# Kernel optimization log

Hardware: AMD Instinct MI355X
Metric: run time of the kernel (lower is better)

The kernel has to match this reference:

```python
import jax, jax.numpy as jnp
import numpy as np

N_NODES = 100000
N_EDGES = 600000
D = 128          # embedding_dim == hidden_dim
OUT = 128        # output_dim
L = 5            # number of GINConv layers


def setup_inputs() -> dict:
    key = jax.random.key(0)
    ks = jax.random.split(key, 9)
    return {
        "x": jax.random.randint(ks[0], (N_NODES,), 0, N_NODES),
        "edge_index": jax.random.randint(ks[1], (2, N_EDGES), 0, N_NODES),
        "emb": jax.random.normal(ks[2], (N_NODES, D), dtype=jnp.float32) * 0.02,
        "Wa": jax.random.normal(ks[3], (L, D, D), dtype=jnp.float32) * 0.05,
        "ba": jnp.zeros((L, D), dtype=jnp.float32),
        "Wb": jax.random.normal(ks[4], (L, D, D), dtype=jnp.float32) * 0.05,
        "bb": jnp.zeros((L, D), dtype=jnp.float32),
        "Wlin": jax.random.normal(ks[5], (D, OUT), dtype=jnp.float32) * 0.05,
        "blin": jnp.zeros((OUT,), dtype=jnp.float32),
    }


def reference(x, edge_index, emb, Wa, ba, Wb, bb, Wlin, blin):
    src, dst = edge_index[0], edge_index[1]
    h = emb[x]  # [N, D] embedding lookup
    for l in range(L):
        # GINConv with eps=0: mlp((1+eps)*x_i + sum_{j->i} x_j)
        agg = jax.ops.segment_sum(h[src], dst, num_segments=N_NODES)  # [N, D]
        z = h + agg
        z = jax.nn.relu(z @ Wa[l] + ba[l])  # MLP hidden
        z = z @ Wb[l] + bb[l]               # MLP out
        h = jax.nn.relu(z)                  # outer F.relu in forward
    pooled = jnp.sum(h, axis=0, keepdims=True)  # global_add_pool, batch=None -> [1, D]
    return pooled @ Wlin + blin                  # [1, OUT]
```

## Files before the change

kernel.cpp:

```cpp
#include <hip/hip_runtime.h>

#define D 128
#define NLAYERS 5

using short8  = __attribute__((ext_vector_type(8))) short;
using short4v = __attribute__((ext_vector_type(4))) short;
using floatx4 = __attribute__((ext_vector_type(4))) float;
using floatx2 = __attribute__((ext_vector_type(2))) float;

__device__ __forceinline__ unsigned bf16_rne(float x) {
    unsigned u = __float_as_uint(x);
    return (u + 0x7fffu + ((u >> 16) & 1u)) >> 16;
}
__device__ __forceinline__ float bf16_to_f32(short s) {
    return __uint_as_float(((unsigned)(unsigned short)s) << 16);
}

#define HSCALE 16.0f
#define HSCALE_INV 0.0625f

__global__ void prepA_kernel(const int* __restrict__ x, const float* __restrict__ emb,
                             const float* __restrict__ Wa, const float* __restrict__ Wb,
                             const int* __restrict__ edst,
                             unsigned char* __restrict__ H0, short* __restrict__ wt,
                             int* __restrict__ deg,
                             int n_nodes, int n_edges) {
    const int gtid = blockIdx.x * 256 + threadIdx.x;
    const int gsz  = gridDim.x * 256;
    for (int g = gtid; g < 2 * NLAYERS * D * D; g += gsz) {
        int mat = g >> 14, idx = g & 16383;
        int n = idx >> 7, k = idx & 127;
        const float* W = (mat & 1) ? (Wb + (size_t)(mat >> 1) * D * D)
                                   : (Wa + (size_t)(mat >> 1) * D * D);
        wt[g] = (short)bf16_rne(W[k * D + n]);
    }
    for (int t = gtid; t < n_nodes * 32; t += gsz) {
        int node = t >> 5, lane = t & 31;
        int s = x[node];
        const float4 v = *reinterpret_cast<const float4*>(emb + (size_t)s * D + lane * 4);
        int w = __builtin_amdgcn_cvt_pk_fp8_f32(v.x * HSCALE, v.y * HSCALE, 0, false);
        w = __builtin_amdgcn_cvt_pk_fp8_f32(v.z * HSCALE, v.w * HSCALE, w, true);
        reinterpret_cast<unsigned int*>(H0)[(size_t)node * 32 + lane] = (unsigned int)w;
    }
    for (int e = gtid; e < n_edges; e += gsz) atomicAdd(&deg[edst[e]], 1);
}

#define SCAN_TILE 1024
__global__ void scan_sums_kernel(const int* __restrict__ deg, int* __restrict__ bsums, int n) {
    __shared__ int red[256];
    int base = blockIdx.x * SCAN_TILE + threadIdx.x * 4;
    int s = 0;
    #pragma unroll
    for (int j = 0; j < 4; j++) {
        int i = base + j;
        if (i < n) s += deg[i];
    }
    red[threadIdx.x] = s;
    __syncthreads();
    for (int off = 128; off > 0; off >>= 1) {
        if (threadIdx.x < off) red[threadIdx.x] += red[threadIdx.x + off];
        __syncthreads();
    }
    if (threadIdx.x == 0) bsums[blockIdx.x] = red[0];
}

__global__ void scan_bsums_kernel(int* __restrict__ bsums, int nblocks) {
    __shared__ int sdata[256];
    int carry = 0;
    for (int base = 0; base < nblocks; base += 256) {
        int i = base + threadIdx.x;
        int v = (i < nblocks) ? bsums[i] : 0;
        sdata[threadIdx.x] = v;
        __syncthreads();
        for (int off = 1; off < 256; off <<= 1) {
            int t = (threadIdx.x >= off) ? sdata[threadIdx.x - off] : 0;
            __syncthreads();
            sdata[threadIdx.x] += t;
            __syncthreads();
        }
        int incl = sdata[threadIdx.x];
        if (i < nblocks) bsums[i] = carry + incl - v;
        carry += sdata[255];
        __syncthreads();
    }
}

__global__ void scan_final_kernel(const int* __restrict__ deg, const int* __restrict__ bsums,
                                  int* __restrict__ offsets, int* __restrict__ cursor, int n) {
    __shared__ int sdata[256];
    int base = blockIdx.x * SCAN_TILE + threadIdx.x * 4;
    int v[4];
    int s = 0;
    #pragma unroll
    for (int j = 0; j < 4; j++) {
        int i = base + j;
        v[j] = (i < n) ? deg[i] : 0;
        s += v[j];
    }
    sdata[threadIdx.x] = s;
    __syncthreads();
    for (int off = 1; off < 256; off <<= 1) {
        int t = (threadIdx.x >= off) ? sdata[threadIdx.x - off] : 0;
        __syncthreads();
        sdata[threadIdx.x] += t;
        __syncthreads();
    }
    int excl = sdata[threadIdx.x] - s + bsums[blockIdx.x];
    #pragma unroll
    for (int j = 0; j < 4; j++) {
        int i = base + j;
        if (i <= n) offsets[i] = excl;
        if (i < n) cursor[i] = excl;
        excl += v[j];
    }
}

__global__ void fill_kernel(const int* __restrict__ esrc, const int* __restrict__ edst,
                            int* __restrict__ cursor, int* __restrict__ csr_src, int n_edges) {
    int e = blockIdx.x * 256 + threadIdx.x;
    if (e >= n_edges) return;
    int pos = atomicAdd(&cursor[edst[e]], 1);
    csr_src[pos] = esrc[e];
}

__global__ __launch_bounds__(512, 6) void layer_kernel(
        const int* __restrict__ offsets, const int* __restrict__ csr_src,
        const unsigned char* __restrict__ h_in, const short* __restrict__ wta,
        const short* __restrict__ wtb, const float* __restrict__ ba,
        const float* __restrict__ bb, unsigned char* __restrict__ h_out,
        float* __restrict__ pooled_accum, int n_rows) {
    __shared__ __align__(16) short zsh[64 * 128];
    __shared__ __align__(16) short wsh[128 * 128];

    const int tid  = threadIdx.x;
    const int row0 = blockIdx.x * 64;

    #pragma unroll
    for (int i = 0; i < 4; i++) {
        int g = i * 512 + tid;
        int n = g >> 4, c = g & 15;
        int off = (n * 16 + (c ^ (n & 15))) * 8;
        *reinterpret_cast<short8*>(&wsh[off]) =
            *reinterpret_cast<const short8*>(wta + n * D + c * 8);
    }

    {
        const int r  = tid >> 3;
        const int l8 = tid & 7;
        const int gr = row0 + r;
        float acc[16];
        if (gr < n_rows) {
            {
                uint4 w = *reinterpret_cast<const uint4*>(h_in + (size_t)gr * D + l8 * 16);
                unsigned int wd[4] = {w.x, w.y, w.z, w.w};
                #pragma unroll
                for (int k = 0; k < 4; k++) {
                    floatx2 lo = __builtin_amdgcn_cvt_pk_f32_fp8((int)wd[k], false);
                    floatx2 hi = __builtin_amdgcn_cvt_pk_f32_fp8((int)wd[k], true);
                    acc[4 * k]     = lo[0]; acc[4 * k + 1] = lo[1];
                    acc[4 * k + 2] = hi[0]; acc[4 * k + 3] = hi[1];
                }
            }
            int beg = offsets[gr];
            int end = offsets[gr + 1];
            int e = beg;
            for (; e + 3 < end; e += 4) {
                int sA = csr_src[e];
                int sB = csr_src[e + 1];
                int sC = csr_src[e + 2];
                int sD = csr_src[e + 3];
                uint4 wA = *reinterpret_cast<const uint4*>(h_in + (size_t)sA * D + l8 * 16);
                uint4 wB = *reinterpret_cast<const uint4*>(h_in + (size_t)sB * D + l8 * 16);
                uint4 wC = *reinterpret_cast<const uint4*>(h_in + (size_t)sC * D + l8 * 16);
                uint4 wD = *reinterpret_cast<const uint4*>(h_in + (size_t)sD * D + l8 * 16);
                unsigned int da[4] = {wA.x, wA.y, wA.z, wA.w};
                unsigned int db[4] = {wB.x, wB.y, wB.z, wB.w};
                unsigned int dc[4] = {wC.x, wC.y, wC.z, wC.w};
                unsigned int dd[4] = {wD.x, wD.y, wD.z, wD.w};
                #pragma unroll
                for (int k = 0; k < 4; k++) {
                    floatx2 alo = __builtin_amdgcn_cvt_pk_f32_fp8((int)da[k], false);
                    floatx2 ahi = __builtin_amdgcn_cvt_pk_f32_fp8((int)da[k], true);
                    floatx2 blo = __builtin_amdgcn_cvt_pk_f32_fp8((int)db[k], false);
                    floatx2 bhi = __builtin_amdgcn_cvt_pk_f32_fp8((int)db[k], true);
                    floatx2 clo = __builtin_amdgcn_cvt_pk_f32_fp8((int)dc[k], false);
                    floatx2 chi = __builtin_amdgcn_cvt_pk_f32_fp8((int)dc[k], true);
                    floatx2 dlo = __builtin_amdgcn_cvt_pk_f32_fp8((int)dd[k], false);
                    floatx2 dhi = __builtin_amdgcn_cvt_pk_f32_fp8((int)dd[k], true);
                    acc[4 * k]     += (alo[0] + blo[0]) + (clo[0] + dlo[0]);
                    acc[4 * k + 1] += (alo[1] + blo[1]) + (clo[1] + dlo[1]);
                    acc[4 * k + 2] += (ahi[0] + bhi[0]) + (chi[0] + dhi[0]);
                    acc[4 * k + 3] += (ahi[1] + bhi[1]) + (chi[1] + dhi[1]);
                }
            }
            for (; e < end; e++) {
                int sA = csr_src[e];
                uint4 wA = *reinterpret_cast<const uint4*>(h_in + (size_t)sA * D + l8 * 16);
                unsigned int da[4] = {wA.x, wA.y, wA.z, wA.w};
                #pragma unroll
                for (int k = 0; k < 4; k++) {
                    floatx2 alo = __builtin_amdgcn_cvt_pk_f32_fp8((int)da[k], false);
                    floatx2 ahi = __builtin_amdgcn_cvt_pk_f32_fp8((int)da[k], true);
                    acc[4 * k]     += alo[0];
                    acc[4 * k + 1] += alo[1];
                    acc[4 * k + 2] += ahi[0];
                    acc[4 * k + 3] += ahi[1];
                }
            }
        } else {
            #pragma unroll
            for (int j = 0; j < 16; j++) acc[j] = 0.f;
        }
        short8 o0, o1;
        #pragma unroll
        for (int j = 0; j < 8; j++) {
            o0[j] = (short)bf16_rne(acc[j] * HSCALE_INV);
            o1[j] = (short)bf16_rne(acc[8 + j] * HSCALE_INV);
        }
        const int c0i = 2 * l8, c1i = 2 * l8 + 1;
        *reinterpret_cast<short8*>(&zsh[(r * 16 + (c0i ^ (r & 15))) * 8]) = o0;
        *reinterpret_cast<short8*>(&zsh[(r * 16 + (c1i ^ (r & 15))) * 8]) = o1;
    }
    __syncthreads();

    const int lane = tid & 63;
    const int wave = tid >> 6;
    const int wr   = wave >> 1;
    const int wc   = wave & 1;
    const int lm   = lane & 15;
    const int quad = lane >> 4;

    floatx4 acc1[4];
    #pragma unroll
    for (int b = 0; b < 4; b++) acc1[b] = floatx4{0.f, 0.f, 0.f, 0.f};
    {
        const int r = wr * 16 + lm;
        #pragma unroll
        for (int ks = 0; ks < 4; ks++) {
            const int c = ks * 4 + quad;
            short8 av = *reinterpret_cast<const short8*>(&zsh[(r * 16 + (c ^ (r & 15))) * 8]);
            #pragma unroll
            for (int cs = 0; cs < 4; cs++) {
                int nn = wc * 64 + cs * 16 + lm;
                short8 bv = *reinterpret_cast<const short8*>(&wsh[(nn * 16 + (c ^ (nn & 15))) * 8]);
                acc1[cs] = __builtin_amdgcn_mfma_f32_16x16x32_bf16(av, bv, acc1[cs], 0, 0, 0);
            }
        }
    }
    __syncthreads();

    #pragma unroll
    for (int i = 0; i < 4; i++) {
        int g = i * 512 + tid;
        int n = g >> 4, c = g & 15;
        int off = (n * 16 + (c ^ (n & 15))) * 8;
        *reinterpret_cast<short8*>(&wsh[off]) =
            *reinterpret_cast<const short8*>(wtb + n * D + c * 8);
    }

    #pragma unroll
    for (int cs = 0; cs < 4; cs++) {
        int col = wc * 64 + cs * 16 + lm;
        float bva = ba[col];
        int cj = col >> 3, ci = col & 7;
        #pragma unroll
        for (int reg = 0; reg < 4; reg++) {
            int r = wr * 16 + quad * 4 + reg;
            float v = fmaxf(acc1[cs][reg] + bva, 0.f);
            zsh[(r * 16 + (cj ^ (r & 15))) * 8 + ci] = (short)bf16_rne(v);
        }
    }
    __syncthreads();

    floatx4 acc2[4];
    #pragma unroll
    for (int b = 0; b < 4; b++) acc2[b] = floatx4{0.f, 0.f, 0.f, 0.f};
    {
        const int r = wr * 16 + lm;
        #pragma unroll
        for (int ks = 0; ks < 4; ks++) {
            const int c = ks * 4 + quad;
            short8 av = *reinterpret_cast<const short8*>(&zsh[(r * 16 + (c ^ (r & 15))) * 8]);
            #pragma unroll
            for (int cs = 0; cs < 4; cs++) {
                int nn = wc * 64 + cs * 16 + lm;
                short8 bv = *reinterpret_cast<const short8*>(&wsh[(nn * 16 + (c ^ (nn & 15))) * 8]);
                acc2[cs] = __builtin_amdgcn_mfma_f32_16x16x32_bf16(av, bv, acc2[cs], 0, 0, 0);
            }
        }
    }

    float psum[4];
    #pragma unroll
    for (int cs = 0; cs < 4; cs++) {
        int col = wc * 64 + cs * 16 + lm;
        float bvb = bb[col];
        float s = 0.f;
        #pragma unroll
        for (int reg = 0; reg < 4; reg++) {
            int r = row0 + wr * 16 + quad * 4 + reg;
            if (r < n_rows) {
                float v = fmaxf(acc2[cs][reg] + bvb, 0.f);
                if (h_out != nullptr) {
                    float sv = v * HSCALE;
                    int pw = __builtin_amdgcn_cvt_pk_fp8_f32(sv, sv, 0, false);
                    h_out[(size_t)r * D + col] = (unsigned char)(pw & 0xff);
                }
                s += v;
            }
        }
        psum[cs] = s;
    }

    if (pooled_accum != nullptr) {
        __syncthreads();
        float* part = (float*)zsh;
        #pragma unroll
        for (int cs = 0; cs < 4; cs++)
            part[(wr * 4 + quad) * 128 + wc * 64 + cs * 16 + lm] = psum[cs];
        __syncthreads();
        if (tid < 128) {
            float s = 0.f;
            #pragma unroll
            for (int g = 0; g < 16; g++) s += part[g * 128 + tid];
            atomicAdd(&pooled_accum[tid], s);
        }
    }
}

__global__ void final_kernel(const float* __restrict__ pooled, const float* __restrict__ Wlin,
                             const float* __restrict__ blin, float* __restrict__ out) {
    const int j = threadIdx.x;
    __shared__ float p[D];
    p[j] = pooled[j];
    __syncthreads();
    float s = blin[j];
    #pragma unroll 8
    for (int k = 0; k < D; k++) s += p[k] * Wlin[k * D + j];
    out[j] = s;
}

extern "C" void kernel_launch(void* const* d_in, const int* in_sizes, int n_in,
                              void* d_out, int out_size, void* d_ws, size_t ws_size,
                              hipStream_t stream) {
    const int*   x    = (const int*)d_in[0];
    const int*   ei   = (const int*)d_in[1];
    const float* emb  = (const float*)d_in[2];
    const float* Wa   = (const float*)d_in[3];
    const float* ba   = (const float*)d_in[4];
    const float* Wb   = (const float*)d_in[5];
    const float* bb   = (const float*)d_in[6];
    const float* Wlin = (const float*)d_in[7];
    const float* blin = (const float*)d_in[8];
    float* out = (float*)d_out;

    const int N = in_sizes[0];
    const int E = in_sizes[1] / 2;
    const int* esrc = ei;
    const int* edst = ei + E;

    unsigned char* H0 = (unsigned char*)d_ws;
    unsigned char* H1 = H0 + (size_t)N * D;
    float* pooled = (float*)(H1 + (size_t)N * D);
    int* deg     = (int*)(pooled + 128);
    int* offsets = deg + N;
    int* cursor  = offsets + (N + 1);
    int* bsums   = cursor + N;
    int* csr_src = bsums + 4096;
    uintptr_t wt_addr = ((uintptr_t)(csr_src + E) + 15) & ~(uintptr_t)15;
    short* wt = (short*)wt_addr;

    const int scan_blocks = (N + 1 + SCAN_TILE - 1) / SCAN_TILE;

    hipMemsetAsync(pooled, 0, (size_t)(128 + N) * sizeof(int), stream);

    prepA_kernel<<<1024, 256, 0, stream>>>(x, emb, Wa, Wb, edst, H0, wt, deg, N, E);
    scan_sums_kernel<<<scan_blocks, 256, 0, stream>>>(deg, bsums, N);
    scan_bsums_kernel<<<1, 256, 0, stream>>>(bsums, scan_blocks);
    scan_final_kernel<<<scan_blocks, 256, 0, stream>>>(deg, bsums, offsets, cursor, N);
    fill_kernel<<<(E + 255) / 256, 256, 0, stream>>>(esrc, edst, cursor, csr_src, E);

    const int layer_blocks = (N + 63) / 64;
    unsigned char* hin = H0; unsigned char* hout = H1;
    for (int l = 0; l < NLAYERS; l++) {
        const bool last = (l == NLAYERS - 1);
        float* pacc = last ? pooled : nullptr;
        unsigned char* hdst = last ? nullptr : hout;
        layer_kernel<<<layer_blocks, 512, 0, stream>>>(
            offsets, csr_src, hin,
            wt + (size_t)(2 * l) * D * D, wt + (size_t)(2 * l + 1) * D * D,
            ba + (size_t)l * D, bb + (size_t)l * D, hdst, pacc, N);
        unsigned char* tmp = hin; hin = hout; hout = tmp;
    }

    final_kernel<<<1, 128, 0, stream>>>(pooled, Wlin, blin, out);
}
```

Before: 379.2 us.

## Split fused layer kernel into separate aggregation and MLP kernels

Moves the neighbor gather-sum out of the fused layer kernel into its own lightweight kernel that writes swizzled bf16 rows to a global z buffer. The MLP kernel then loads those tiles straight into shared memory. The intent is to let the latency-bound gather run at higher occupancy, free of the MLP's shared-memory and register limits. The cost is an extra global write and read of an N×128 bf16 intermediate per layer, plus an extra launch per layer.

```diff
diff --git a/kernel.cpp b/kernel.cpp
--- a/kernel.cpp
+++ b/kernel.cpp
@@ -123,9 +123,84 @@
     csr_src[pos] = esrc[e];
 }
 
-__global__ __launch_bounds__(512, 6) void layer_kernel(
+__global__ __launch_bounds__(256) void agg_kernel(
         const int* __restrict__ offsets, const int* __restrict__ csr_src,
-        const unsigned char* __restrict__ h_in, const short* __restrict__ wta,
+        const unsigned char* __restrict__ h_in, short* __restrict__ z, int n_rows) {
+    const int t   = blockIdx.x * 256 + threadIdx.x;
+    const int row = t >> 3;
+    const int l8  = t & 7;
+    if (row >= n_rows) return;
+
+    float acc[16];
+    {
+        uint4 w = *reinterpret_cast<const uint4*>(h_in + (size_t)row * D + l8 * 16);
+        unsigned int wd[4] = {w.x, w.y, w.z, w.w};
+        #pragma unroll
+        for (int k = 0; k < 4; k++) {
+            floatx2 lo = __builtin_amdgcn_cvt_pk_f32_fp8((int)wd[k], false);
+            floatx2 hi = __builtin_amdgcn_cvt_pk_f32_fp8((int)wd[k], true);
+            acc[4 * k]     = lo[0]; acc[4 * k + 1] = lo[1];
+            acc[4 * k + 2] = hi[0]; acc[4 * k + 3] = hi[1];
+        }
+    }
+    int e   = offsets[row];
+    int end = offsets[row + 1];
+    for (; e + 3 < end; e += 4) {
+        int sA = csr_src[e];
+        int sB = csr_src[e + 1];
+        int sC = csr_src[e + 2];
+        int sD = csr_src[e + 3];
+        uint4 wA = *reinterpret_cast<const uint4*>(h_in + (size_t)sA * D + l8 * 16);
+        uint4 wB = *reinterpret_cast<const uint4*>(h_in + (size_t)sB * D + l8 * 16);
+        uint4 wC = *reinterpret_cast<const uint4*>(h_in + (size_t)sC * D + l8 * 16);
+        uint4 wD = *reinterpret_cast<const uint4*>(h_in + (size_t)sD * D + l8 * 16);
+        unsigned int da[4] = {wA.x, wA.y, wA.z, wA.w};
+        unsigned int db[4] = {wB.x, wB.y, wB.z, wB.w};
+        unsigned int dc[4] = {wC.x, wC.y, wC.z, wC.w};
+        unsigned int dd[4] = {wD.x, wD.y, wD.z, wD.w};
+        #pragma unroll
+        for (int k = 0; k < 4; k++) {
+            floatx2 alo = __builtin_amdgcn_cvt_pk_f32_fp8((int)da[k], false);
+            floatx2 ahi = __builtin_amdgcn_cvt_pk_f32_fp8((int)da[k], true);
+            floatx2 blo = __builtin_amdgcn_cvt_pk_f32_fp8((int)db[k], false);
+            floatx2 bhi = __builtin_amdgcn_cvt_pk_f32_fp8((int)db[k], true);
+            floatx2 clo = __builtin_amdgcn_cvt_pk_f32_fp8((int)dc[k], false);
+            floatx2 chi = __builtin_amdgcn_cvt_pk_f32_fp8((int)dc[k], true);
+            floatx2 dlo = __builtin_amdgcn_cvt_pk_f32_fp8((int)dd[k], false);
+            floatx2 dhi = __builtin_amdgcn_cvt_pk_f32_fp8((int)dd[k], true);
+            acc[4 * k]     += (alo[0] + blo[0]) + (clo[0] + dlo[0]);
+            acc[4 * k + 1] += (alo[1] + blo[1]) + (clo[1] + dlo[1]);
+            acc[4 * k + 2] += (ahi[0] + bhi[0]) + (chi[0] + dhi[0]);
+            acc[4 * k + 3] += (ahi[1] + bhi[1]) + (chi[1] + dhi[1]);
+        }
+    }
+    for (; e < end; e++) {
+        int sA = csr_src[e];
+        uint4 wA = *reinterpret_cast<const uint4*>(h_in + (size_t)sA * D + l8 * 16);
+        unsigned int da[4] = {wA.x, wA.y, wA.z, wA.w};
+        #pragma unroll
+        for (int k = 0; k < 4; k++) {
+            floatx2 alo = __builtin_amdgcn_cvt_pk_f32_fp8((int)da[k], false);
+            floatx2 ahi = __builtin_amdgcn_cvt_pk_f32_fp8((int)da[k], true);
+            acc[4 * k]     += alo[0];
+            acc[4 * k + 1] += alo[1];
+            acc[4 * k + 2] += ahi[0];
+            acc[4 * k + 3] += ahi[1];
+        }
+    }
+    short8 o0, o1;
+    #pragma unroll
+    for (int j = 0; j < 8; j++) {
+        o0[j] = (short)bf16_rne(acc[j] * HSCALE_INV);
+        o1[j] = (short)bf16_rne(acc[8 + j] * HSCALE_INV);
+    }
+    const int c0 = 2 * l8, c1 = 2 * l8 + 1;
+    *reinterpret_cast<short8*>(z + ((size_t)row * 16 + (c0 ^ (row & 15))) * 8) = o0;
+    *reinterpret_cast<short8*>(z + ((size_t)row * 16 + (c1 ^ (row & 15))) * 8) = o1;
+}
+
+__global__ __launch_bounds__(512, 6) void mlp_kernel(
+        const short* __restrict__ z, const short* __restrict__ wta,
         const short* __restrict__ wtb, const float* __restrict__ ba,
         const float* __restrict__ bb, unsigned char* __restrict__ h_out,
         float* __restrict__ pooled_accum, int n_rows) {
@@ -143,83 +218,16 @@
         *reinterpret_cast<short8*>(&wsh[off]) =
             *reinterpret_cast<const short8*>(wta + n * D + c * 8);
     }
-
-    {
-        const int r  = tid >> 3;
-        const int l8 = tid & 7;
-        const int gr = row0 + r;
-        float acc[16];
-        if (gr < n_rows) {
-            {
-                uint4 w = *reinterpret_cast<const uint4*>(h_in + (size_t)gr * D + l8 * 16);
-                unsigned int wd[4] = {w.x, w.y, w.z, w.w};
-                #pragma unroll
-                for (int k = 0; k < 4; k++) {
-                    floatx2 lo = __builtin_amdgcn_cvt_pk_f32_fp8((int)wd[k], false);
-                    floatx2 hi = __builtin_amdgcn_cvt_pk_f32_fp8((int)wd[k], true);
-                    acc[4 * k]     = lo[0]; acc[4 * k + 1] = lo[1];
-                    acc[4 * k + 2] = hi[0]; acc[4 * k + 3] = hi[1];
-                }
-            }
-            int beg = offsets[gr];
-            int end = offsets[gr + 1];
-            int e = beg;
-            for (; e + 3 < end; e += 4) {
-                int sA = csr_src[e];
-                int sB = csr_src[e + 1];
-                int sC = csr_src[e + 2];
-                int sD = csr_src[e + 3];
-                uint4 wA = *reinterpret_cast<const uint4*>(h_in + (size_t)sA * D + l8 * 16);
-                uint4 wB = *reinterpret_cast<const uint4*>(h_in + (size_t)sB * D + l8 * 16);
-                uint4 wC = *reinterpret_cast<const uint4*>(h_in + (size_t)sC * D + l8 * 16);
-                uint4 wD = *reinterpret_cast<const uint4*>(h_in + (size_t)sD * D + l8 * 16);
-                unsigned int da[4] = {wA.x, wA.y, wA.z, wA.w};
-                unsigned int db[4] = {wB.x, wB.y, wB.z, wB.w};
-                unsigned int dc[4] = {wC.x, wC.y, wC.z, wC.w};
-                unsigned int dd[4] = {wD.x, wD.y, wD.z, wD.w};
-                #pragma unroll
-                for (int k = 0; k < 4; k++) {
-                    floatx2 alo = __builtin_amdgcn_cvt_pk_f32_fp8((int)da[k], false);
-                    floatx2 ahi = __builtin_amdgcn_cvt_pk_f32_fp8((int)da[k], true);
-                    floatx2 blo = __builtin_amdgcn_cvt_pk_f32_fp8((int)db[k], false);
-                    floatx2 bhi = __builtin_amdgcn_cvt_pk_f32_fp8((int)db[k], true);
-                    floatx2 clo = __builtin_amdgcn_cvt_pk_f32_fp8((int)dc[k], false);
-                    floatx2 chi = __builtin_amdgcn_cvt_pk_f32_fp8((int)dc[k], true);
-                    floatx2 dlo = __builtin_amdgcn_cvt_pk_f32_fp8((int)dd[k], false);
-                    floatx2 dhi = __builtin_amdgcn_cvt_pk_f32_fp8((int)dd[k], true);
-                    acc[4 * k]     += (alo[0] + blo[0]) + (clo[0] + dlo[0]);
-                    acc[4 * k + 1] += (alo[1] + blo[1]) + (clo[1] + dlo[1]);
-                    acc[4 * k + 2] += (ahi[0] + bhi[0]) + (chi[0] + dhi[0]);
-                    acc[4 * k + 3] += (ahi[1] + bhi[1]) + (chi[1] + dhi[1]);
-                }
-            }
-            for (; e < end; e++) {
-                int sA = csr_src[e];
-                uint4 wA = *reinterpret_cast<const uint4*>(h_in + (size_t)sA * D + l8 * 16);
-                unsigned int da[4] = {wA.x, wA.y, wA.z, wA.w};
-                #pragma unroll
-                for (int k = 0; k < 4; k++) {
-                    floatx2 alo = __builtin_amdgcn_cvt_pk_f32_fp8((int)da[k], false);
-                    floatx2 ahi = __builtin_amdgcn_cvt_pk_f32_fp8((int)da[k], true);
-                    acc[4 * k]     += alo[0];
-                    acc[4 * k + 1] += alo[1];
-                    acc[4 * k + 2] += ahi[0];
-                    acc[4 * k + 3] += ahi[1];
-                }
-            }
-        } else {
-            #pragma unroll
-            for (int j = 0; j < 16; j++) acc[j] = 0.f;
-        }
-        short8 o0, o1;
-        #pragma unroll
-        for (int j = 0; j < 8; j++) {
-            o0[j] = (short)bf16_rne(acc[j] * HSCALE_INV);
-            o1[j] = (short)bf16_rne(acc[8 + j] * HSCALE_INV);
-        }
-        const int c0i = 2 * l8, c1i = 2 * l8 + 1;
-        *reinterpret_cast<short8*>(&zsh[(r * 16 + (c0i ^ (r & 15))) * 8]) = o0;
-        *reinterpret_cast<short8*>(&zsh[(r * 16 + (c1i ^ (r & 15))) * 8]) = o1;
+    #pragma unroll
+    for (int i = 0; i < 2; i++) {
+        int idx = i * 512 + tid;
+        int r = idx >> 4;
+        short8 v;
+        if (row0 + r < n_rows)
+            v = *reinterpret_cast<const short8*>(z + ((size_t)row0 * 16 + idx) * 8);
+        else
+            v = short8{0, 0, 0, 0, 0, 0, 0, 0};
+        *reinterpret_cast<short8*>(&zsh[idx * 8]) = v;
     }
     __syncthreads();
 
@@ -361,7 +369,8 @@
 
     unsigned char* H0 = (unsigned char*)d_ws;
     unsigned char* H1 = H0 + (size_t)N * D;
-    float* pooled = (float*)(H1 + (size_t)N * D);
+    short* zbuf = (short*)(H1 + (size_t)N * D);
+    float* pooled = (float*)(zbuf + (size_t)N * D);
     int* deg     = (int*)(pooled + 128);
     int* offsets = deg + N;
     int* cursor  = offsets + (N + 1);
@@ -380,15 +389,16 @@
     scan_final_kernel<<<scan_blocks, 256, 0, stream>>>(deg, bsums, offsets, cursor, N);
     fill_kernel<<<(E + 255) / 256, 256, 0, stream>>>(esrc, edst, cursor, csr_src, E);
 
-    const int layer_blocks = (N + 63) / 64;
+    const int agg_blocks = (N * 8 + 255) / 256;
+    const int mlp_blocks = (N + 63) / 64;
     unsigned char* hin = H0; unsigned char* hout = H1;
     for (int l = 0; l < NLAYERS; l++) {
         const bool last = (l == NLAYERS - 1);
         float* pacc = last ? pooled : nullptr;
         unsigned char* hdst = last ? nullptr : hout;
-        layer_kernel<<<layer_blocks, 512, 0, stream>>>(
-            offsets, csr_src, hin,
-            wt + (size_t)(2 * l) * D * D, wt + (size_t)(2 * l + 1) * D * D,
+        agg_kernel<<<agg_blocks, 256, 0, stream>>>(offsets, csr_src, hin, zbuf, N);
+        mlp_kernel<<<mlp_blocks, 512, 0, stream>>>(
+            zbuf, wt + (size_t)(2 * l) * D * D, wt + (size_t)(2 * l + 1) * D * D,
             ba + (size_t)l * D, bb + (size_t)l * D, hdst, pacc, N);
         unsigned char* tmp = hin; hin = hout; hout = tmp;
     }
```

After: 415.4 us. 9.5% more time.
